# Performance work log

Measured on AMD Instinct MI355X. Metric: run time of the kernel, lower is better.

The kernel has to match this reference:

```python
import jax, jax.numpy as jnp
import numpy as np

MAT_MODE = [(0, 1), (0, 2), (1, 2)]
VEC_MODE = [2, 1, 0]
AABB_LO = -1.5
INV_SIZE = 2.0 / 3.0  # 2 / (hi - lo) with aabb [-1.5, 1.5]


def _bilinear2d(plane, gx, gy):
    # plane: [C,H,W]; gx,gy: [N] in [-1,1]; align_corners=True, zero padding
    C, H, W = plane.shape
    ix = (gx + 1.0) * 0.5 * (W - 1)
    iy = (gy + 1.0) * 0.5 * (H - 1)
    x0 = jnp.floor(ix).astype(jnp.int32)
    y0 = jnp.floor(iy).astype(jnp.int32)
    x1, y1 = x0 + 1, y0 + 1
    wx1 = ix - x0
    wy1 = iy - y0
    wx0 = 1.0 - wx1
    wy0 = 1.0 - wy1

    def gather(xi, yi, w):
        valid = (xi >= 0) & (xi < W) & (yi >= 0) & (yi < H)
        xc = jnp.clip(xi, 0, W - 1)
        yc = jnp.clip(yi, 0, H - 1)
        return plane[:, yc, xc] * (w * valid)  # [C,N]

    return (gather(x0, y0, wx0 * wy0) + gather(x1, y0, wx1 * wy0)
            + gather(x0, y1, wx0 * wy1) + gather(x1, y1, wx1 * wy1))


def _linear1d(line, gz):
    # line: [C,L]; gz: [N] in [-1,1]; matches grid_sample on [C,L,1] with x=0
    C, L = line.shape
    iz = (gz + 1.0) * 0.5 * (L - 1)
    z0 = jnp.floor(iz).astype(jnp.int32)
    z1 = z0 + 1
    w1 = iz - z0
    w0 = 1.0 - w1

    def gather(zi, w):
        valid = (zi >= 0) & (zi < L)
        zc = jnp.clip(zi, 0, L - 1)
        return line[:, zc] * (w * valid)  # [C,N]

    return gather(z0, w0) + gather(z1, w1)


def setup_inputs() -> dict:
    key = jax.random.key(0)
    ks = jax.random.split(key, 9)
    N, J, C, G = 262144, 24, 16, 128
    xyz = jax.random.uniform(ks[0], (N, 3), jnp.float32) * 2.0 - 1.0
    transforms = (jnp.eye(4, dtype=jnp.float32)[None]
                  + 0.05 * jax.random.normal(ks[1], (J, 4, 4), jnp.float32))
    scale = 0.032
    planes = [scale * jax.random.normal(ks[2 + i], (J, C, G, G), jnp.float32) for i in range(3)]
    lines = [scale * jax.random.normal(ks[5 + i], (J, C, G), jnp.float32) for i in range(3)]
    return {"xyz": xyz, "transforms": transforms,
            "plane0": planes[0], "plane1": planes[1], "plane2": planes[2],
            "line0": lines[0], "line1": lines[1], "line2": lines[2]}


def reference(xyz, transforms, plane0, plane1, plane2, line0, line1, line2):
    # compute_weights: per-joint transform of homogeneous points
    N = xyz.shape[0]
    xyz_h = jnp.concatenate([xyz, jnp.ones((N, 1), xyz.dtype)], axis=-1)  # [N,4]
    pts = jnp.einsum('jab,nb->jna', transforms, xyz_h)[..., :3]           # [J,N,3]
    g = (pts - AABB_LO) * INV_SIZE - 1.0                                  # normalize_coord
    g = jax.lax.stop_gradient(g)  # torch .detach() on sampling coords

    planes = (plane0, plane1, plane2)
    lines = (line0, line1, line2)
    J = transforms.shape[0]
    sigma = jnp.zeros((J, N), xyz.dtype)
    for p in range(3):
        m0, m1 = MAT_MODE[p]
        v = VEC_MODE[p]
        pf = jax.vmap(_bilinear2d)(planes[p], g[..., m0], g[..., m1])  # [J,C,N]
        lf = jax.vmap(_linear1d)(lines[p], g[..., v])                  # [J,C,N]
        sigma = sigma + jnp.sum(pf * lf, axis=1)
    return jax.nn.relu(sigma).T  # weights [N,J]
```

## Files before the change

### kernel.cpp

```cpp
#include <hip/hip_runtime.h>
#include <hip/hip_fp16.h>

#define NPTS 262144
#define NJ   24
#define NC   16
#define NG   128
#define PSZ  (NJ*NG*NG*NC)
#define LSZ  (NJ*NG*NC)
#define NBIN 32768

typedef _Float16 h2 __attribute__((ext_vector_type(2)));
typedef _Float16 h8 __attribute__((ext_vector_type(8)));

static __device__ __forceinline__ h8 splat8(float w) {
    _Float16 h = (_Float16)w;
    return (h8){h,h,h,h,h,h,h,h};
}

#define OFF_WSP   ((size_t)0)
#define OFF_WSL   (OFF_WSP + (size_t)3*PSZ*2)
#define OFF_OUTT  (OFF_WSL + (size_t)3*LSZ*2)
#define OFF_PERM  (OFF_OUTT + (size_t)NJ*NPTS*2)
#define OFF_XYZS  (OFF_PERM + (size_t)NPTS*4)
#define OFF_HIST  (OFF_XYZS + (size_t)NPTS*16)
#define OFF_CUR   (OFF_HIST + (size_t)NBIN*4)
#define WS_NEED   (OFF_CUR + (size_t)NBIN*4)


__global__ __launch_bounds__(256) void transpose_planes_c(
    const float* __restrict__ p0, const float* __restrict__ p1,
    const float* __restrict__ p2, _Float16* __restrict__ wsP)
{
    const int p = blockIdx.z, j = blockIdx.y;
    const int x = threadIdx.x & 127;
    const int y = blockIdx.x * 2 + (threadIdx.x >> 7);
    const float* src = ((p == 0) ? p0 : (p == 1) ? p1 : p2)
                     + ((size_t)j * NC * NG + y) * NG + x;
    _Float16 v[16];
#pragma unroll
    for (int c = 0; c < NC; ++c)
        v[c] = (_Float16)src[(size_t)c * NG * NG];
    _Float16* dst = wsP + (size_t)p * PSZ + (size_t)((j * NG + y) * NG + x) * NC;
    *(h8*)dst       = (h8){v[0],v[1],v[2],v[3],v[4],v[5],v[6],v[7]};
    *(h8*)(dst + 8) = (h8){v[8],v[9],v[10],v[11],v[12],v[13],v[14],v[15]};
}

__global__ __launch_bounds__(256) void transpose_lines_h(
    const float* __restrict__ l0, const float* __restrict__ l1,
    const float* __restrict__ l2, _Float16* __restrict__ wsL)
{
    const int p = blockIdx.z;
    const int idx = blockIdx.x * 256 + threadIdx.x;
    const int c = idx & 15;
    const int z = (idx >> 4) & 127;
    const int j = idx >> 11;
    const float* src = (p == 0) ? l0 : (p == 1) ? l1 : l2;
    wsL[(size_t)p * LSZ + (size_t)(j * NG + z) * NC + c] =
        (_Float16)src[(j * NC + c) * NG + z];
}


static __device__ __forceinline__ int bin_key(float x, float y, float z) {
    const int qx = min(max((int)((x + 1.0f) * 16.0f), 0), 31);
    const int qy = min(max((int)((y + 1.0f) * 16.0f), 0), 31);
    const int qz = min(max((int)((z + 1.0f) * 16.0f), 0), 31);
    int k = 0;
#pragma unroll
    for (int b = 0; b < 5; ++b) {
        k |= (((qx >> b) & 1) << (3*b + 2))
           | (((qy >> b) & 1) << (3*b + 1))
           | (((qz >> b) & 1) << (3*b));
    }
    return k;
}

__global__ __launch_bounds__(256) void hist_k(
    const float* __restrict__ xyz, int* __restrict__ hist)
{
    const int n = blockIdx.x * 256 + threadIdx.x;
    atomicAdd(&hist[bin_key(xyz[3*n], xyz[3*n+1], xyz[3*n+2])], 1);
}

__global__ __launch_bounds__(256) void scan_k(
    const int* __restrict__ hist, int* __restrict__ cursor)
{
    __shared__ int ssum[256];
    const int tid = threadIdx.x;
    const int base = tid * 128;
    int s = 0;
    for (int k = 0; k < 128; ++k) s += hist[base + k];
    ssum[tid] = s;
    __syncthreads();
    for (int off = 1; off < 256; off <<= 1) {
        int v = (tid >= off) ? ssum[tid - off] : 0;
        __syncthreads();
        ssum[tid] += v;
        __syncthreads();
    }
    int run = (tid == 0) ? 0 : ssum[tid - 1];
    for (int k = 0; k < 128; ++k) {
        cursor[base + k] = run;
        run += hist[base + k];
    }
}

__global__ __launch_bounds__(256) void scatter_k(
    const float* __restrict__ xyz, int* __restrict__ cursor,
    int* __restrict__ perm, float* __restrict__ xyzS )
{
    const int n = blockIdx.x * 256 + threadIdx.x;
    const float x = xyz[3*n], y = xyz[3*n+1], z = xyz[3*n+2];
    const int pos = atomicAdd(&cursor[bin_key(x, y, z)], 1);
    perm[pos] = n;
    *(float4*)(xyzS + 4*(size_t)pos) = make_float4(x, y, z, 0.0f);
}


__global__ __launch_bounds__(256) void trisample_s_k(
    const float* __restrict__ xyzS, const float* __restrict__ Tm,
    const _Float16* __restrict__ wsP, const _Float16* __restrict__ wsL,
    _Float16* __restrict__ outT )
{
    __shared__ _Float16 sL[3 * NG * NC];

    const int sb = (blockIdx.x & 7) * (49152 >> 3) + (blockIdx.x >> 3);
    const int j  = sb >> 11;
    const int s0 = (sb & 2047) << 7;

    {
        uint4* s4 = (uint4*)sL;
#pragma unroll
        for (int k = 0; k < 3; ++k) {
            const int idx = k * 256 + threadIdx.x;
            const int p = idx >> 8, r = idx & 255;
            s4[idx] = ((const uint4*)(wsL + (size_t)p * LSZ + (size_t)j * (NG*NC)))[r];
        }
    }
    __syncthreads();

    const int s  = s0 + (threadIdx.x >> 1);
    const int hh = (threadIdx.x & 1) << 3;

    const float4 pv = *(const float4*)(xyzS + 4*(size_t)s);
    const float px = pv.x, py = pv.y, pz = pv.z;
    const float* Tj = Tm + 16*j;

    float m0[3], m1[3];
    int   c0[3], c1[3];
#pragma unroll
    for (int a = 0; a < 3; ++a) {
        const float pt = fmaf(Tj[4*a+0], px,
                          fmaf(Tj[4*a+1], py,
                           fmaf(Tj[4*a+2], pz, Tj[4*a+3])));
        const float ia = fmaf(pt, 127.0f/3.0f, 63.5f);
        const float fa = floorf(ia);
        const int   i0 = (int)fa;
        const float w1 = ia - fa;
        m0[a] = (i0 >=  0 && i0 < NG    ) ? (1.0f - w1) : 0.0f;
        m1[a] = (i0 >= -1 && i0 < NG - 1) ? w1          : 0.0f;
        c0[a] = min(max(i0,     0), NG-1);
        c1[a] = min(max(i0 + 1, 0), NG-1);
    }

    const int M0[3] = {0,0,1}, M1[3] = {1,2,2}, MV[3] = {2,1,0};

    const _Float16* pbase[3];
    int rb0[3], rb1[3], cb0[3], cb1[3];
#pragma unroll
    for (int p = 0; p < 3; ++p) {
        pbase[p] = wsP + (size_t)p * PSZ + (size_t)j * (NG*NG*NC) + hh;
        rb0[p] = c0[M1[p]] * (NG*NC);  rb1[p] = c1[M1[p]] * (NG*NC);
        cb0[p] = c0[M0[p]] * NC;       cb1[p] = c1[M0[p]] * NC;
    }

    float sigma = 0.0f;
    h8 a0 = *(const h8*)(pbase[0] + rb0[0] + cb0[0]);
    h8 a1 = *(const h8*)(pbase[0] + rb0[0] + cb1[0]);
    h8 a2 = *(const h8*)(pbase[0] + rb1[0] + cb0[0]);
    h8 a3 = *(const h8*)(pbase[0] + rb1[0] + cb1[0]);
#pragma unroll
    for (int p = 0; p < 3; ++p) {
        h8 b0, b1, b2, b3;
        if (p < 2) {
            b0 = *(const h8*)(pbase[p+1] + rb0[p+1] + cb0[p+1]);
            b1 = *(const h8*)(pbase[p+1] + rb0[p+1] + cb1[p+1]);
            b2 = *(const h8*)(pbase[p+1] + rb1[p+1] + cb0[p+1]);
            b3 = *(const h8*)(pbase[p+1] + rb1[p+1] + cb1[p+1]);
        }
        const int A = M0[p], B = M1[p], V = MV[p];
        const h8 u0 = *(const h8*)(sL + (p * NG + c0[V]) * NC + hh);
        const h8 u1 = *(const h8*)(sL + (p * NG + c1[V]) * NC + hh);

        h8 pf = a0 * splat8(m0[A] * m0[B]);
        pf += a1 * splat8(m1[A] * m0[B]);
        pf += a2 * splat8(m0[A] * m1[B]);
        pf += a3 * splat8(m1[A] * m1[B]);
        h8 lf = u0 * splat8(m0[V]);
        lf += u1 * splat8(m1[V]);

#if __has_builtin(__builtin_amdgcn_fdot2)
#pragma unroll
        for (int q = 0; q < 4; ++q) {
            const h2 va = {pf[2*q], pf[2*q+1]};
            const h2 vb = {lf[2*q], lf[2*q+1]};
            sigma = __builtin_amdgcn_fdot2(va, vb, sigma, false);
        }
#else
#pragma unroll
        for (int q = 0; q < 8; ++q)
            sigma += (float)pf[q] * (float)lf[q];
#endif
        if (p < 2) { a0 = b0; a1 = b1; a2 = b2; a3 = b3; }
    }

    sigma += __shfl_xor(sigma, 1);
    if (hh == 0)
        outT[(size_t)j * NPTS + s] = (_Float16)fmaxf(sigma, 0.0f);
}


__global__ __launch_bounds__(256) void finalize_k(
    const _Float16* __restrict__ outT, const int* __restrict__ perm,
    float* __restrict__ out)
{
    const int s = blockIdx.x * 256 + threadIdx.x;
    const int n = perm[s];
    float4 o[6];
#pragma unroll
    for (int j = 0; j < NJ; ++j)
        ((float*)o)[j] = (float)outT[(size_t)j * NPTS + s];
    float4* dst = (float4*)(out + (size_t)n * NJ);
#pragma unroll
    for (int k = 0; k < 6; ++k) dst[k] = o[k];
}


__global__ __launch_bounds__(256) void simple_trisample_k(
    const float* __restrict__ xyz, const float* __restrict__ Tm,
    const float* __restrict__ p0, const float* __restrict__ p1,
    const float* __restrict__ p2, const float* __restrict__ l0,
    const float* __restrict__ l1, const float* __restrict__ l2,
    float* __restrict__ out)
{
    const int tid = blockIdx.x * 256 + threadIdx.x;
    const int j = tid >> 18;
    const int n = tid & (NPTS - 1);
    const float x = xyz[3*n+0], y = xyz[3*n+1], z = xyz[3*n+2];
    const float* Tj = Tm + 16*j;
    float g[3];
#pragma unroll
    for (int a = 0; a < 3; ++a) {
        const float pt = Tj[4*a+0]*x + Tj[4*a+1]*y + Tj[4*a+2]*z + Tj[4*a+3];
        g[a] = (pt + 1.5f) * (2.0f/3.0f) - 1.0f;
    }
    const float* P[3] = {p0, p1, p2};
    const float* L[3] = {l0, l1, l2};
    const int M0[3] = {0,0,1}, M1[3] = {1,2,2}, MV[3] = {2,1,0};
    float sigma = 0.0f;
#pragma unroll
    for (int p = 0; p < 3; ++p) {
        const float ix = (g[M0[p]] + 1.0f) * 63.5f;
        const float iy = (g[M1[p]] + 1.0f) * 63.5f;
        const float iz = (g[MV[p]] + 1.0f) * 63.5f;
        const float fx = floorf(ix), fy = floorf(iy), fz = floorf(iz);
        const int x0 = (int)fx, y0 = (int)fy, z0 = (int)fz;
        const float wx1 = ix - fx, wy1 = iy - fy, wz1 = iz - fz;
        const float mx0 = (x0   >= 0 && x0   < NG) ? (1.0f - wx1) : 0.0f;
        const float mx1 = (x0+1 >= 0 && x0+1 < NG) ? wx1 : 0.0f;
        const float my0 = (y0   >= 0 && y0   < NG) ? (1.0f - wy1) : 0.0f;
        const float my1 = (y0+1 >= 0 && y0+1 < NG) ? wy1 : 0.0f;
        const float mz0 = (z0   >= 0 && z0   < NG) ? (1.0f - wz1) : 0.0f;
        const float mz1 = (z0+1 >= 0 && z0+1 < NG) ? wz1 : 0.0f;
        const int xc0 = min(max(x0,0),NG-1), xc1 = min(max(x0+1,0),NG-1);
        const int yc0 = min(max(y0,0),NG-1), yc1 = min(max(y0+1,0),NG-1);
        const int zc0 = min(max(z0,0),NG-1), zc1 = min(max(z0+1,0),NG-1);
        const float w00 = mx0*my0, w01 = mx1*my0, w10 = mx0*my1, w11 = mx1*my1;
        const int o00 = yc0*NG+xc0, o01 = yc0*NG+xc1, o10 = yc1*NG+xc0, o11 = yc1*NG+xc1;
        const float* pb = P[p] + (size_t)j * NC * NG * NG;
        const float* lb = L[p] + (size_t)j * NC * NG;
#pragma unroll 4
        for (int c = 0; c < NC; ++c) {
            const float* pc = pb + (size_t)c * NG * NG;
            const float pf = pc[o00]*w00 + pc[o01]*w01 + pc[o10]*w10 + pc[o11]*w11;
            const float* lc = lb + (size_t)c * NG;
            sigma += pf * (lc[zc0]*mz0 + lc[zc1]*mz1);
        }
    }
    out[(size_t)n * NJ + j] = fmaxf(sigma, 0.0f);
}


extern "C" void kernel_launch(void* const* d_in, const int* in_sizes, int n_in,
                              void* d_out, int out_size, void* d_ws, size_t ws_size,
                              hipStream_t stream) {
    const float* xyz = nullptr;
    const float* Tm  = nullptr;
    const float* P[3] = {nullptr, nullptr, nullptr};
    const float* L[3] = {nullptr, nullptr, nullptr};
    int pi = 0, li = 0;
    for (int i = 0; i < n_in; ++i) {
        const int si = in_sizes[i];
        if      (si == NPTS * 3)            xyz = (const float*)d_in[i];
        else if (si == 16 * NJ)             Tm  = (const float*)d_in[i];
        else if (si == NJ * NC * NG * NG) { if (pi < 3) P[pi++] = (const float*)d_in[i]; }
        else if (si == NJ * NC * NG)      { if (li < 3) L[li++] = (const float*)d_in[i]; }
    }
    if (!xyz || !Tm || pi != 3 || li != 3) {
        xyz = (const float*)d_in[0];  Tm = (const float*)d_in[1];
        P[0] = (const float*)d_in[2]; P[1] = (const float*)d_in[3];
        P[2] = (const float*)d_in[4];
        L[0] = (const float*)d_in[5]; L[1] = (const float*)d_in[6];
        L[2] = (const float*)d_in[7];
    }
    float* out = (float*)d_out;
    char*  ws  = (char*)d_ws;

    if (ws_size >= WS_NEED) {
        _Float16* wsP   = (_Float16*)(ws + OFF_WSP);
        _Float16* wsL   = (_Float16*)(ws + OFF_WSL);
        _Float16* outT  = (_Float16*)(ws + OFF_OUTT);
        int*      perm  = (int*)     (ws + OFF_PERM);
        float*    xyzS  = (float*)   (ws + OFF_XYZS);
        int*      hist  = (int*)     (ws + OFF_HIST);
        int*      cur   = (int*)     (ws + OFF_CUR);

        hipMemsetAsync(hist, 0, (size_t)2 * NBIN * sizeof(int), stream);
        transpose_planes_c<<<dim3(NG/2, NJ, 3), 256, 0, stream>>>(P[0], P[1], P[2], wsP);
        transpose_lines_h<<<dim3(LSZ/256, 1, 3), 256, 0, stream>>>(L[0], L[1], L[2], wsL);
        hist_k<<<NPTS/256, 256, 0, stream>>>(xyz, hist);
        scan_k<<<1, 256, 0, stream>>>(hist, cur);
        scatter_k<<<NPTS/256, 256, 0, stream>>>(xyz, cur, perm, xyzS);
        trisample_s_k<<<49152, 256, 0, stream>>>(xyzS, Tm, wsP, wsL, outT);
        finalize_k<<<NPTS/256, 256, 0, stream>>>(outT, perm, out);
    } else {
        simple_trisample_k<<<(NPTS*NJ)/256, 256, 0, stream>>>(xyz, Tm, P[0], P[1], P[2],
                                                              L[0], L[1], L[2], out);
    }
}
```

Baseline: 190.5 us.

## Fuse prep kernels and make trisample blocks loop over multiple point chunks

Merges the plane transpose, line transpose and histogram kernels into one launch, dispatched by block-index ranges. The plane transpose now reads float2 pairs so each thread writes two texels. The sampling kernel has each block handle 1024 sorted points in 8 chunks instead of 128, so the per-block shared-memory line staging is paid 8x less often and the grid shrinks to 6144 blocks. The trade-off is fewer blocks to hide latency and longer per-block serial work.

```diff
diff --git a/kernel.cpp b/kernel.cpp
--- a/kernel.cpp
+++ b/kernel.cpp
@@ -27,39 +27,6 @@
 #define WS_NEED   (OFF_CUR + (size_t)NBIN*4)
 
 
-__global__ __launch_bounds__(256) void transpose_planes_c(
-    const float* __restrict__ p0, const float* __restrict__ p1,
-    const float* __restrict__ p2, _Float16* __restrict__ wsP)
-{
-    const int p = blockIdx.z, j = blockIdx.y;
-    const int x = threadIdx.x & 127;
-    const int y = blockIdx.x * 2 + (threadIdx.x >> 7);
-    const float* src = ((p == 0) ? p0 : (p == 1) ? p1 : p2)
-                     + ((size_t)j * NC * NG + y) * NG + x;
-    _Float16 v[16];
-#pragma unroll
-    for (int c = 0; c < NC; ++c)
-        v[c] = (_Float16)src[(size_t)c * NG * NG];
-    _Float16* dst = wsP + (size_t)p * PSZ + (size_t)((j * NG + y) * NG + x) * NC;
-    *(h8*)dst       = (h8){v[0],v[1],v[2],v[3],v[4],v[5],v[6],v[7]};
-    *(h8*)(dst + 8) = (h8){v[8],v[9],v[10],v[11],v[12],v[13],v[14],v[15]};
-}
-
-__global__ __launch_bounds__(256) void transpose_lines_h(
-    const float* __restrict__ l0, const float* __restrict__ l1,
-    const float* __restrict__ l2, _Float16* __restrict__ wsL)
-{
-    const int p = blockIdx.z;
-    const int idx = blockIdx.x * 256 + threadIdx.x;
-    const int c = idx & 15;
-    const int z = (idx >> 4) & 127;
-    const int j = idx >> 11;
-    const float* src = (p == 0) ? l0 : (p == 1) ? l1 : l2;
-    wsL[(size_t)p * LSZ + (size_t)(j * NG + z) * NC + c] =
-        (_Float16)src[(j * NC + c) * NG + z];
-}
-
-
 static __device__ __forceinline__ int bin_key(float x, float y, float z) {
     const int qx = min(max((int)((x + 1.0f) * 16.0f), 0), 31);
     const int qy = min(max((int)((y + 1.0f) * 16.0f), 0), 31);
@@ -74,11 +41,55 @@
     return k;
 }
 
-__global__ __launch_bounds__(256) void hist_k(
-    const float* __restrict__ xyz, int* __restrict__ hist)
-{
-    const int n = blockIdx.x * 256 + threadIdx.x;
-    atomicAdd(&hist[bin_key(xyz[3*n], xyz[3*n+1], xyz[3*n+2])], 1);
+
+#define PB_P 2304
+#define PB_L 576
+#define PB_H 1024
+#define PB_TOT (PB_P + PB_L + PB_H)
+
+__global__ __launch_bounds__(256) void prep_k(
+    const float* __restrict__ p0, const float* __restrict__ p1,
+    const float* __restrict__ p2, const float* __restrict__ l0,
+    const float* __restrict__ l1, const float* __restrict__ l2,
+    const float* __restrict__ xyz, _Float16* __restrict__ wsP,
+    _Float16* __restrict__ wsL, int* __restrict__ hist)
+{
+    const int b = blockIdx.x;
+    if (b < PB_P) {
+        const int p   = b / 768;
+        const int rem = b % 768;
+        const int j   = rem >> 5;
+        const int x = (threadIdx.x & 63) * 2;
+        const int y = (rem & 31) * 4 + (threadIdx.x >> 6);
+        const float* src = ((p == 0) ? p0 : (p == 1) ? p1 : p2)
+                         + ((size_t)j * NC * NG + y) * NG + x;
+        float2 v[16];
+#pragma unroll
+        for (int c = 0; c < NC; ++c)
+            v[c] = *(const float2*)(src + (size_t)c * NG * NG);
+        _Float16* dst = wsP + (size_t)p * PSZ + (size_t)((j * NG + y) * NG + x) * NC;
+        *(h8*)(dst)      = (h8){(_Float16)v[0].x,(_Float16)v[1].x,(_Float16)v[2].x,(_Float16)v[3].x,
+                                (_Float16)v[4].x,(_Float16)v[5].x,(_Float16)v[6].x,(_Float16)v[7].x};
+        *(h8*)(dst + 8)  = (h8){(_Float16)v[8].x,(_Float16)v[9].x,(_Float16)v[10].x,(_Float16)v[11].x,
+                                (_Float16)v[12].x,(_Float16)v[13].x,(_Float16)v[14].x,(_Float16)v[15].x};
+        *(h8*)(dst + 16) = (h8){(_Float16)v[0].y,(_Float16)v[1].y,(_Float16)v[2].y,(_Float16)v[3].y,
+                                (_Float16)v[4].y,(_Float16)v[5].y,(_Float16)v[6].y,(_Float16)v[7].y};
+        *(h8*)(dst + 24) = (h8){(_Float16)v[8].y,(_Float16)v[9].y,(_Float16)v[10].y,(_Float16)v[11].y,
+                                (_Float16)v[12].y,(_Float16)v[13].y,(_Float16)v[14].y,(_Float16)v[15].y};
+    } else if (b < PB_P + PB_L) {
+        const int t = b - PB_P;
+        const int p = t / 192;
+        const int idx = (t % 192) * 256 + threadIdx.x;
+        const int c = idx & 15;
+        const int z = (idx >> 4) & 127;
+        const int j = idx >> 11;
+        const float* src = (p == 0) ? l0 : (p == 1) ? l1 : l2;
+        wsL[(size_t)p * LSZ + (size_t)(j * NG + z) * NC + c] =
+            (_Float16)src[(j * NC + c) * NG + z];
+    } else {
+        const int n = (b - PB_P - PB_L) * 256 + threadIdx.x;
+        atomicAdd(&hist[bin_key(xyz[3*n], xyz[3*n+1], xyz[3*n+2])], 1);
+    }
 }
 
 __global__ __launch_bounds__(256) void scan_k(
@@ -116,16 +127,16 @@
 }
 
 
-__global__ __launch_bounds__(256) void trisample_s_k(
+__global__ __launch_bounds__(256) void trisample_m_k(
     const float* __restrict__ xyzS, const float* __restrict__ Tm,
     const _Float16* __restrict__ wsP, const _Float16* __restrict__ wsL,
     _Float16* __restrict__ outT )
 {
     __shared__ _Float16 sL[3 * NG * NC];
 
-    const int sb = (blockIdx.x & 7) * (49152 >> 3) + (blockIdx.x >> 3);
-    const int j  = sb >> 11;
-    const int s0 = (sb & 2047) << 7;
+    const int sb = (blockIdx.x & 7) * 768 + (blockIdx.x >> 3);
+    const int j  = sb >> 8;
+    const int g0 = (sb & 255) << 10;
 
     {
         uint4* s4 = (uint4*)sL;
@@ -138,84 +149,91 @@
     }
     __syncthreads();
 
-    const int s  = s0 + (threadIdx.x >> 1);
-    const int hh = (threadIdx.x & 1) << 3;
-
-    const float4 pv = *(const float4*)(xyzS + 4*(size_t)s);
-    const float px = pv.x, py = pv.y, pz = pv.z;
+    const int sbase = g0 + (threadIdx.x >> 1);
+    const int hh    = (threadIdx.x & 1) << 3;
     const float* Tj = Tm + 16*j;
-
-    float m0[3], m1[3];
-    int   c0[3], c1[3];
-#pragma unroll
-    for (int a = 0; a < 3; ++a) {
-        const float pt = fmaf(Tj[4*a+0], px,
-                          fmaf(Tj[4*a+1], py,
-                           fmaf(Tj[4*a+2], pz, Tj[4*a+3])));
-        const float ia = fmaf(pt, 127.0f/3.0f, 63.5f);
-        const float fa = floorf(ia);
-        const int   i0 = (int)fa;
-        const float w1 = ia - fa;
-        m0[a] = (i0 >=  0 && i0 < NG    ) ? (1.0f - w1) : 0.0f;
-        m1[a] = (i0 >= -1 && i0 < NG - 1) ? w1          : 0.0f;
-        c0[a] = min(max(i0,     0), NG-1);
-        c1[a] = min(max(i0 + 1, 0), NG-1);
-    }
-
     const int M0[3] = {0,0,1}, M1[3] = {1,2,2}, MV[3] = {2,1,0};
 
-    const _Float16* pbase[3];
-    int rb0[3], rb1[3], cb0[3], cb1[3];
-#pragma unroll
-    for (int p = 0; p < 3; ++p) {
-        pbase[p] = wsP + (size_t)p * PSZ + (size_t)j * (NG*NG*NC) + hh;
-        rb0[p] = c0[M1[p]] * (NG*NC);  rb1[p] = c1[M1[p]] * (NG*NC);
-        cb0[p] = c0[M0[p]] * NC;       cb1[p] = c1[M0[p]] * NC;
-    }
-
-    float sigma = 0.0f;
-    h8 a0 = *(const h8*)(pbase[0] + rb0[0] + cb0[0]);
-    h8 a1 = *(const h8*)(pbase[0] + rb0[0] + cb1[0]);
-    h8 a2 = *(const h8*)(pbase[0] + rb1[0] + cb0[0]);
-    h8 a3 = *(const h8*)(pbase[0] + rb1[0] + cb1[0]);
-#pragma unroll
-    for (int p = 0; p < 3; ++p) {
-        h8 b0, b1, b2, b3;
-        if (p < 2) {
-            b0 = *(const h8*)(pbase[p+1] + rb0[p+1] + cb0[p+1]);
-            b1 = *(const h8*)(pbase[p+1] + rb0[p+1] + cb1[p+1]);
-            b2 = *(const h8*)(pbase[p+1] + rb1[p+1] + cb0[p+1]);
-            b3 = *(const h8*)(pbase[p+1] + rb1[p+1] + cb1[p+1]);
-        }
-        const int A = M0[p], B = M1[p], V = MV[p];
-        const h8 u0 = *(const h8*)(sL + (p * NG + c0[V]) * NC + hh);
-        const h8 u1 = *(const h8*)(sL + (p * NG + c1[V]) * NC + hh);
-
-        h8 pf = a0 * splat8(m0[A] * m0[B]);
-        pf += a1 * splat8(m1[A] * m0[B]);
-        pf += a2 * splat8(m0[A] * m1[B]);
-        pf += a3 * splat8(m1[A] * m1[B]);
-        h8 lf = u0 * splat8(m0[V]);
-        lf += u1 * splat8(m1[V]);
+    const _Float16* pjbase[3];
+#pragma unroll
+    for (int p = 0; p < 3; ++p)
+        pjbase[p] = wsP + (size_t)p * PSZ + (size_t)j * (NG*NG*NC) + hh;
+
+#pragma unroll 4
+    for (int ch = 0; ch < 8; ++ch) {
+        const int s = sbase + (ch << 7);
+
+        const float4 pv = *(const float4*)(xyzS + 4*(size_t)s);
+        const float px = pv.x, py = pv.y, pz = pv.z;
+
+        float m0[3], m1[3];
+        int   c0[3], c1[3];
+#pragma unroll
+        for (int a = 0; a < 3; ++a) {
+            const float pt = fmaf(Tj[4*a+0], px,
+                              fmaf(Tj[4*a+1], py,
+                               fmaf(Tj[4*a+2], pz, Tj[4*a+3])));
+            const float ia = fmaf(pt, 127.0f/3.0f, 63.5f);
+            const float fa = floorf(ia);
+            const int   i0 = (int)fa;
+            const float w1 = ia - fa;
+            m0[a] = (i0 >=  0 && i0 < NG    ) ? (1.0f - w1) : 0.0f;
+            m1[a] = (i0 >= -1 && i0 < NG - 1) ? w1          : 0.0f;
+            c0[a] = min(max(i0,     0), NG-1);
+            c1[a] = min(max(i0 + 1, 0), NG-1);
+        }
+
+        int rb0[3], rb1[3], cb0[3], cb1[3];
+#pragma unroll
+        for (int p = 0; p < 3; ++p) {
+            rb0[p] = c0[M1[p]] * (NG*NC);  rb1[p] = c1[M1[p]] * (NG*NC);
+            cb0[p] = c0[M0[p]] * NC;       cb1[p] = c1[M0[p]] * NC;
+        }
+
+        float sigma = 0.0f;
+        h8 a0 = *(const h8*)(pjbase[0] + rb0[0] + cb0[0]);
+        h8 a1 = *(const h8*)(pjbase[0] + rb0[0] + cb1[0]);
+        h8 a2 = *(const h8*)(pjbase[0] + rb1[0] + cb0[0]);
+        h8 a3 = *(const h8*)(pjbase[0] + rb1[0] + cb1[0]);
+#pragma unroll
+        for (int p = 0; p < 3; ++p) {
+            h8 b0, b1, b2, b3;
+            if (p < 2) {
+                b0 = *(const h8*)(pjbase[p+1] + rb0[p+1] + cb0[p+1]);
+                b1 = *(const h8*)(pjbase[p+1] + rb0[p+1] + cb1[p+1]);
+                b2 = *(const h8*)(pjbase[p+1] + rb1[p+1] + cb0[p+1]);
+                b3 = *(const h8*)(pjbase[p+1] + rb1[p+1] + cb1[p+1]);
+            }
+            const int A = M0[p], B = M1[p], V = MV[p];
+            const h8 u0 = *(const h8*)(sL + (p * NG + c0[V]) * NC + hh);
+            const h8 u1 = *(const h8*)(sL + (p * NG + c1[V]) * NC + hh);
+
+            h8 pf = a0 * splat8(m0[A] * m0[B]);
+            pf += a1 * splat8(m1[A] * m0[B]);
+            pf += a2 * splat8(m0[A] * m1[B]);
+            pf += a3 * splat8(m1[A] * m1[B]);
+            h8 lf = u0 * splat8(m0[V]);
+            lf += u1 * splat8(m1[V]);
 
 #if __has_builtin(__builtin_amdgcn_fdot2)
 #pragma unroll
-        for (int q = 0; q < 4; ++q) {
-            const h2 va = {pf[2*q], pf[2*q+1]};
-            const h2 vb = {lf[2*q], lf[2*q+1]};
-            sigma = __builtin_amdgcn_fdot2(va, vb, sigma, false);
-        }
+            for (int q = 0; q < 4; ++q) {
+                const h2 va = {pf[2*q], pf[2*q+1]};
+                const h2 vb = {lf[2*q], lf[2*q+1]};
+                sigma = __builtin_amdgcn_fdot2(va, vb, sigma, false);
+            }
 #else
 #pragma unroll
-        for (int q = 0; q < 8; ++q)
-            sigma += (float)pf[q] * (float)lf[q];
+            for (int q = 0; q < 8; ++q)
+                sigma += (float)pf[q] * (float)lf[q];
 #endif
-        if (p < 2) { a0 = b0; a1 = b1; a2 = b2; a3 = b3; }
-    }
-
-    sigma += __shfl_xor(sigma, 1);
-    if (hh == 0)
-        outT[(size_t)j * NPTS + s] = (_Float16)fmaxf(sigma, 0.0f);
+            if (p < 2) { a0 = b0; a1 = b1; a2 = b2; a3 = b3; }
+        }
+
+        sigma += __shfl_xor(sigma, 1);
+        if (hh == 0)
+            outT[(size_t)j * NPTS + s] = (_Float16)fmaxf(sigma, 0.0f);
+    }
 }
 
 
@@ -325,12 +343,11 @@
         int*      cur   = (int*)     (ws + OFF_CUR);
 
         hipMemsetAsync(hist, 0, (size_t)2 * NBIN * sizeof(int), stream);
-        transpose_planes_c<<<dim3(NG/2, NJ, 3), 256, 0, stream>>>(P[0], P[1], P[2], wsP);
-        transpose_lines_h<<<dim3(LSZ/256, 1, 3), 256, 0, stream>>>(L[0], L[1], L[2], wsL);
-        hist_k<<<NPTS/256, 256, 0, stream>>>(xyz, hist);
+        prep_k<<<PB_TOT, 256, 0, stream>>>(P[0], P[1], P[2], L[0], L[1], L[2],
+                                           xyz, wsP, wsL, hist);
         scan_k<<<1, 256, 0, stream>>>(hist, cur);
         scatter_k<<<NPTS/256, 256, 0, stream>>>(xyz, cur, perm, xyzS);
-        trisample_s_k<<<49152, 256, 0, stream>>>(xyzS, Tm, wsP, wsL, outT);
+        trisample_m_k<<<6144, 256, 0, stream>>>(xyzS, Tm, wsP, wsL, outT);
         finalize_k<<<NPTS/256, 256, 0, stream>>>(outT, perm, out);
     } else {
         simple_trisample_k<<<(NPTS*NJ)/256, 256, 0, stream>>>(xyz, Tm, P[0], P[1], P[2],
```

New measurement: 177.7 us. 1.07x faster.
